# Kernel tuning notes

Hardware: AMD Instinct MI355X
Metric: run time of the kernel (lower is better)

The kernel has to match this reference:

```python
import jax, jax.numpy as jnp
import numpy as np

EMBED_DIM = 32
HIDDEN_DIM = 64


def setup_inputs() -> dict:
    key = jax.random.key(0)
    B, N = 16, 512
    k1, k2, k3 = jax.random.split(key, 3)
    node_emb = jax.random.normal(k1, (B * N, EMBED_DIM), dtype=jnp.float32)
    # MLP params: Linear(2*embed_dim -> hidden), Linear(hidden -> 1)
    s1 = 1.0 / np.sqrt(2 * EMBED_DIM)
    s2 = 1.0 / np.sqrt(HIDDEN_DIM)
    W1 = jax.random.uniform(k2, (2 * EMBED_DIM, HIDDEN_DIM), minval=-s1, maxval=s1, dtype=jnp.float32)
    b1 = jnp.zeros((HIDDEN_DIM,), dtype=jnp.float32)
    W2 = jax.random.uniform(k3, (HIDDEN_DIM, 1), minval=-s2, maxval=s2, dtype=jnp.float32)
    b2 = jnp.zeros((1,), dtype=jnp.float32)
    return {"node_emb": node_emb, "W1": W1, "b1": b1, "W2": W2, "b2": b2, "B": B, "N": N}


def reference(node_emb, W1, b1, W2, b2, B, N):
    E = node_emb.shape[1]
    H = node_emb.reshape(B, N, E)
    # upper-triangular (i<j) node pairs, matching itertools.combinations order
    idx_i, idx_j = jnp.triu_indices(N, k=1)          # (P,), P = N*(N-1)/2
    h_i = H[:, idx_i]                                 # (B, P, E)
    h_j = H[:, idx_j]                                 # (B, P, E)
    h_cat = jnp.concatenate([h_i, h_j], axis=-1)      # (B, P, 2E)
    h = jax.nn.relu(jnp.einsum('bpe,eh->bph', h_cat, W1) + b1)
    prob = jax.nn.sigmoid(jnp.einsum('bph,ho->bpo', h, W2) + b2)[..., 0]  # (B, P)
    adj = jnp.zeros((B, N, N), dtype=prob.dtype).at[:, idx_i, idx_j].set(prob)
    return adj + adj.transpose(0, 2, 1)
```

## Files before the change

kernel.cpp:

```cpp
#include <hip/hip_runtime.h>
#include <math.h>

#define NN   512
#define BB   16
#define EMB  32
#define HID  64
#define TILE 64
#define LDSP 68

__global__ __launch_bounds__(256) void precompute_uv(
    const float* __restrict__ emb, const float* __restrict__ W1,
    const float* __restrict__ b1, float* __restrict__ u, float* __restrict__ v)
{
    int g = blockIdx.x * 256 + threadIdx.x;
    int n = g >> 6, h = g & 63;
    const float* Hrow = emb + n * EMB;
    float su = b1[h];
    float sv = 0.f;
    #pragma unroll
    for (int e = 0; e < EMB; ++e) {
        float he = Hrow[e];
        su = fmaf(he, W1[e * HID + h], su);
        sv = fmaf(he, W1[(e + EMB) * HID + h], sv);
    }
    u[n * HID + h] = su;
    v[n * HID + h] = sv;
}

__global__ __launch_bounds__(256) void edge_tile(
    const float* __restrict__ u, const float* __restrict__ v,
    const float* __restrict__ W2, const float* __restrict__ b2p,
    float* __restrict__ out)
{
    int bj = blockIdx.x, bi = blockIdx.y, b = blockIdx.z;
    if (bi > bj) return;

    __shared__ __align__(16) float u_s[TILE][LDSP];
    __shared__ __align__(16) float v_s[TILE][LDSP];

    int t = threadIdx.x;

    const float* ubase = u + ((size_t)b * NN + bi * TILE) * HID;
    const float* vbase = v + ((size_t)b * NN + bj * TILE) * HID;
    {
        int row  = t >> 4;
        int col  = (t & 15) * 4;
        #pragma unroll
        for (int p = 0; p < 4; ++p) {
            int rr = row + p * 16;
            *(float4*)&u_s[rr][col] = *(const float4*)&ubase[rr * HID + col];
            *(float4*)&v_s[rr][col] = *(const float4*)&vbase[rr * HID + col];
        }
    }
    __syncthreads();

    int tr = t >> 4;
    int tc = t & 15;

    float acc[4][4];
    #pragma unroll
    for (int i = 0; i < 4; ++i)
        #pragma unroll
        for (int j = 0; j < 4; ++j) acc[i][j] = 0.f;

    const float4* w2v = (const float4*)W2;
    #pragma unroll 4
    for (int h4 = 0; h4 < 16; ++h4) {
        float4 a[4], bv[4];
        #pragma unroll
        for (int k = 0; k < 4; ++k) a[k]  = *(const float4*)&u_s[tr + 16*k][h4 * 4];
        #pragma unroll
        for (int k = 0; k < 4; ++k) bv[k] = *(const float4*)&v_s[tc + 16*k][h4 * 4];
        float4 w = w2v[h4];
        #pragma unroll
        for (int i = 0; i < 4; ++i)
            #pragma unroll
            for (int j = 0; j < 4; ++j) {
                float x0 = fmaxf(a[i].x + bv[j].x, 0.f);
                float x1 = fmaxf(a[i].y + bv[j].y, 0.f);
                float x2 = fmaxf(a[i].z + bv[j].z, 0.f);
                float x3 = fmaxf(a[i].w + bv[j].w, 0.f);
                acc[i][j] = fmaf(x0, w.x, acc[i][j]);
                acc[i][j] = fmaf(x1, w.y, acc[i][j]);
                acc[i][j] = fmaf(x2, w.z, acc[i][j]);
                acc[i][j] = fmaf(x3, w.w, acc[i][j]);
            }
    }

    float b2 = b2p[0];
    float val[4][4];
    #pragma unroll
    for (int i = 0; i < 4; ++i)
        #pragma unroll
        for (int j = 0; j < 4; ++j) {
            float x = acc[i][j] + b2;
            val[i][j] = 1.f / (1.f + __expf(-x));
        }

    float* res = &u_s[0][0];

    if (bi != bj) {
        float* obase = out + (size_t)b * NN * NN + (size_t)(bi * TILE) * NN + bj * TILE;
        #pragma unroll
        for (int i = 0; i < 4; ++i) {
            int r = tr + 16 * i;
            #pragma unroll
            for (int j = 0; j < 4; ++j)
                obase[r * NN + tc + 16 * j] = val[i][j];
        }
        __syncthreads();
        #pragma unroll
        for (int i = 0; i < 4; ++i)
            #pragma unroll
            for (int j = 0; j < 4; ++j)
                res[(tc + 16 * j) * LDSP + (tr + 16 * i)] = val[i][j];
        __syncthreads();
        float* obase2 = out + (size_t)b * NN * NN + (size_t)(bj * TILE) * NN + bi * TILE;
        int row  = t >> 2;
        int col0 = (t & 3) * 16;
        #pragma unroll
        for (int q = 0; q < 4; ++q)
            *(float4*)&obase2[row * NN + col0 + q * 4] =
                *(const float4*)&res[row * LDSP + col0 + q * 4];
    } else {
        __syncthreads();
        #pragma unroll
        for (int i = 0; i < 4; ++i)
            #pragma unroll
            for (int j = 0; j < 4; ++j)
                res[(tr + 16 * i) * LDSP + (tc + 16 * j)] = val[i][j];
        __syncthreads();
        float* obase = out + (size_t)b * NN * NN + (size_t)(bi * TILE) * NN + bj * TILE;
        int row  = t >> 2;
        int col0 = (t & 3) * 16;
        for (int q = 0; q < 16; ++q) {
            int c = col0 + q;
            float x;
            if (row == c)      x = 0.f;
            else if (row < c)  x = res[row * LDSP + c];
            else               x = res[c * LDSP + row];
            obase[row * NN + c] = x;
        }
    }
}

extern "C" void kernel_launch(void* const* d_in, const int* in_sizes, int n_in,
                              void* d_out, int out_size, void* d_ws, size_t ws_size,
                              hipStream_t stream) {
    const float* emb = (const float*)d_in[0];
    const float* W1  = (const float*)d_in[1];
    const float* b1  = (const float*)d_in[2];
    const float* W2  = (const float*)d_in[3];
    const float* b2  = (const float*)d_in[4];
    float* outp = (float*)d_out;

    float* uu = (float*)d_ws;
    float* vv = uu + (size_t)BB * NN * HID;

    precompute_uv<<<dim3((BB * NN * HID) / 256), 256, 0, stream>>>(emb, W1, b1, uu, vv);

    dim3 grid(NN / TILE, NN / TILE, BB);
    edge_tile<<<grid, 256, 0, stream>>>(uu, vv, W2, b2, outp);
}
```

Before: 103.5 us.

## Store u/v in fp16 and use packed fp16 add/max with fdot2 accumulation

```diff
diff --git a/kernel.cpp b/kernel.cpp
--- a/kernel.cpp
+++ b/kernel.cpp
@@ -6,11 +6,14 @@
 #define EMB  32
 #define HID  64
 #define TILE 64
-#define LDSP 68
+#define ROWD 36
+#define RST  68
+
+typedef _Float16 h2 __attribute__((ext_vector_type(2)));
 
 __global__ __launch_bounds__(256) void precompute_uv(
     const float* __restrict__ emb, const float* __restrict__ W1,
-    const float* __restrict__ b1, float* __restrict__ u, float* __restrict__ v)
+    const float* __restrict__ b1, _Float16* __restrict__ u, _Float16* __restrict__ v)
 {
     int g = blockIdx.x * 256 + threadIdx.x;
     int n = g >> 6, h = g & 63;
@@ -23,36 +26,47 @@
         su = fmaf(he, W1[e * HID + h], su);
         sv = fmaf(he, W1[(e + EMB) * HID + h], sv);
     }
-    u[n * HID + h] = su;
-    v[n * HID + h] = sv;
+    u[n * HID + h] = (_Float16)su;
+    v[n * HID + h] = (_Float16)sv;
 }
 
 __global__ __launch_bounds__(256) void edge_tile(
-    const float* __restrict__ u, const float* __restrict__ v,
+    const _Float16* __restrict__ u, const _Float16* __restrict__ v,
     const float* __restrict__ W2, const float* __restrict__ b2p,
     float* __restrict__ out)
 {
     int bj = blockIdx.x, bi = blockIdx.y, b = blockIdx.z;
     if (bi > bj) return;
 
-    __shared__ __align__(16) float u_s[TILE][LDSP];
-    __shared__ __align__(16) float v_s[TILE][LDSP];
+    __shared__ __align__(16) float smem[2 * TILE * ROWD];
+    __shared__ float w2s[HID / 2];
+    float* u_s = smem;
+    float* v_s = smem + TILE * ROWD;
+    float* res = smem;
 
     int t = threadIdx.x;
 
-    const float* ubase = u + ((size_t)b * NN + bi * TILE) * HID;
-    const float* vbase = v + ((size_t)b * NN + bj * TILE) * HID;
+    const _Float16* ubase = u + ((size_t)b * NN + bi * TILE) * HID;
+    const _Float16* vbase = v + ((size_t)b * NN + bj * TILE) * HID;
     {
-        int row  = t >> 4;
-        int col  = (t & 15) * 4;
         #pragma unroll
-        for (int p = 0; p < 4; ++p) {
-            int rr = row + p * 16;
-            *(float4*)&u_s[rr][col] = *(const float4*)&ubase[rr * HID + col];
-            *(float4*)&v_s[rr][col] = *(const float4*)&vbase[rr * HID + col];
+        for (int p = 0; p < 2; ++p) {
+            int idx = t + p * 256;
+            int row = idx >> 3, c4 = idx & 7;
+            *(float4*)&u_s[row * ROWD + c4 * 4] = *(const float4*)&ubase[row * HID + c4 * 8];
+            *(float4*)&v_s[row * ROWD + c4 * 4] = *(const float4*)&vbase[row * HID + c4 * 8];
+        }
+        if (t < 32) {
+            float2 w = ((const float2*)W2)[t];
+            h2 hw = { (_Float16)w.x, (_Float16)w.y };
+            w2s[t] = __builtin_bit_cast(float, hw);
         }
     }
     __syncthreads();
+
+    float4 w2f[8];
+    #pragma unroll
+    for (int q = 0; q < 8; ++q) w2f[q] = *(const float4*)&w2s[q * 4];
 
     int tr = t >> 4;
     int tc = t & 15;
@@ -63,28 +77,34 @@
         #pragma unroll
         for (int j = 0; j < 4; ++j) acc[i][j] = 0.f;
 
-    const float4* w2v = (const float4*)W2;
-    #pragma unroll 4
-    for (int h4 = 0; h4 < 16; ++h4) {
+    const h2 hz = { (_Float16)0.f, (_Float16)0.f };
+
+    #pragma unroll
+    for (int h8 = 0; h8 < 8; ++h8) {
         float4 a[4], bv[4];
         #pragma unroll
-        for (int k = 0; k < 4; ++k) a[k]  = *(const float4*)&u_s[tr + 16*k][h4 * 4];
+        for (int k = 0; k < 4; ++k) a[k]  = *(const float4*)&u_s[(tr + 16 * k) * ROWD + h8 * 4];
         #pragma unroll
-        for (int k = 0; k < 4; ++k) bv[k] = *(const float4*)&v_s[tc + 16*k][h4 * 4];
-        float4 w = w2v[h4];
+        for (int k = 0; k < 4; ++k) bv[k] = *(const float4*)&v_s[(tc + 16 * k) * ROWD + h8 * 4];
+        float4 w = w2f[h8];
+        h2 w0 = __builtin_bit_cast(h2, w.x), w1 = __builtin_bit_cast(h2, w.y);
+        h2 w2_ = __builtin_bit_cast(h2, w.z), w3 = __builtin_bit_cast(h2, w.w);
         #pragma unroll
-        for (int i = 0; i < 4; ++i)
+        for (int i = 0; i < 4; ++i) {
+            h2 ax = __builtin_bit_cast(h2, a[i].x), ay = __builtin_bit_cast(h2, a[i].y);
+            h2 az = __builtin_bit_cast(h2, a[i].z), aw = __builtin_bit_cast(h2, a[i].w);
             #pragma unroll
             for (int j = 0; j < 4; ++j) {
-                float x0 = fmaxf(a[i].x + bv[j].x, 0.f);
-                float x1 = fmaxf(a[i].y + bv[j].y, 0.f);
-                float x2 = fmaxf(a[i].z + bv[j].z, 0.f);
-                float x3 = fmaxf(a[i].w + bv[j].w, 0.f);
-                acc[i][j] = fmaf(x0, w.x, acc[i][j]);
-                acc[i][j] = fmaf(x1, w.y, acc[i][j]);
-                acc[i][j] = fmaf(x2, w.z, acc[i][j]);
-                acc[i][j] = fmaf(x3, w.w, acc[i][j]);
+                h2 bx = __builtin_bit_cast(h2, bv[j].x), by = __builtin_bit_cast(h2, bv[j].y);
+                h2 bz = __builtin_bit_cast(h2, bv[j].z), bw = __builtin_bit_cast(h2, bv[j].w);
+                float s = acc[i][j];
+                s = __builtin_amdgcn_fdot2(__builtin_elementwise_max(ax + bx, hz), w0, s, false);
+                s = __builtin_amdgcn_fdot2(__builtin_elementwise_max(ay + by, hz), w1, s, false);
+                s = __builtin_amdgcn_fdot2(__builtin_elementwise_max(az + bz, hz), w2_, s, false);
+                s = __builtin_amdgcn_fdot2(__builtin_elementwise_max(aw + bw, hz), w3, s, false);
+                acc[i][j] = s;
             }
+        }
     }
 
     float b2 = b2p[0];
@@ -97,38 +117,43 @@
             val[i][j] = 1.f / (1.f + __expf(-x));
         }
 
-    float* res = &u_s[0][0];
+    __syncthreads();
+
+    int r16 = t >> 4;
+    int l16 = t & 15;
 
     if (bi != bj) {
-        float* obase = out + (size_t)b * NN * NN + (size_t)(bi * TILE) * NN + bj * TILE;
         #pragma unroll
-        for (int i = 0; i < 4; ++i) {
-            int r = tr + 16 * i;
+        for (int i = 0; i < 4; ++i)
             #pragma unroll
             for (int j = 0; j < 4; ++j)
-                obase[r * NN + tc + 16 * j] = val[i][j];
+                res[(tr + 16 * i) * RST + tc + 16 * j] = val[i][j];
+        __syncthreads();
+        float* o1 = out + (size_t)b * NN * NN + (size_t)(bi * TILE) * NN + bj * TILE;
+        #pragma unroll
+        for (int q = 0; q < 4; ++q) {
+            int r = r16 + q * 16;
+            *(float4*)&o1[(size_t)r * NN + l16 * 4] = *(const float4*)&res[r * RST + l16 * 4];
         }
         __syncthreads();
         #pragma unroll
         for (int i = 0; i < 4; ++i)
             #pragma unroll
             for (int j = 0; j < 4; ++j)
-                res[(tc + 16 * j) * LDSP + (tr + 16 * i)] = val[i][j];
+                res[(tc + 16 * j) * RST + tr + 16 * i] = val[i][j];
         __syncthreads();
-        float* obase2 = out + (size_t)b * NN * NN + (size_t)(bj * TILE) * NN + bi * TILE;
-        int row  = t >> 2;
-        int col0 = (t & 3) * 16;
+        float* o2 = out + (size_t)b * NN * NN + (size_t)(bj * TILE) * NN + bi * TILE;
         #pragma unroll
-        for (int q = 0; q < 4; ++q)
-            *(float4*)&obase2[row * NN + col0 + q * 4] =
-                *(const float4*)&res[row * LDSP + col0 + q * 4];
+        for (int q = 0; q < 4; ++q) {
+            int r = r16 + q * 16;
+            *(float4*)&o2[(size_t)r * NN + l16 * 4] = *(const float4*)&res[r * RST + l16 * 4];
+        }
     } else {
-        __syncthreads();
         #pragma unroll
         for (int i = 0; i < 4; ++i)
             #pragma unroll
             for (int j = 0; j < 4; ++j)
-                res[(tr + 16 * i) * LDSP + (tc + 16 * j)] = val[i][j];
+                res[(tr + 16 * i) * RST + tc + 16 * j] = val[i][j];
         __syncthreads();
         float* obase = out + (size_t)b * NN * NN + (size_t)(bi * TILE) * NN + bj * TILE;
         int row  = t >> 2;
@@ -137,9 +162,9 @@
             int c = col0 + q;
             float x;
             if (row == c)      x = 0.f;
-            else if (row < c)  x = res[row * LDSP + c];
-            else               x = res[c * LDSP + row];
-            obase[row * NN + c] = x;
+            else if (row < c)  x = res[row * RST + c];
+            else               x = res[c * RST + row];
+            obase[(size_t)row * NN + c] = x;
         }
     }
 }
@@ -154,8 +179,8 @@
     const float* b2  = (const float*)d_in[4];
     float* outp = (float*)d_out;
 
-    float* uu = (float*)d_ws;
-    float* vv = uu + (size_t)BB * NN * HID;
+    _Float16* uu = (_Float16*)d_ws;
+    _Float16* vv = uu + (size_t)BB * NN * HID;
 
     precompute_uv<<<dim3((BB * NN * HID) / 256), 256, 0, stream>>>(emb, W1, b1, uu, vv);
 
```

After: 96.54 us. 6.8% less time.
